# Performance work log

Measured on AMD Instinct MI355X. Metric: run time of the kernel, lower is better.

## Reference

```python
import jax, jax.numpy as jnp
import numpy as np

LENS = 0.4
DECAY = 0.2
THRESH = 0.2
LOG_SIG_MIN, LOG_SIG_MAX = -20.0, 2.0

# Surrogate-gradient spike: forward is heaviside, backward is rectangular window |x|<lens
@jax.custom_vjp
def act_fun(x):
    return (x > 0.0).astype(x.dtype)

def _act_fwd(x):
    return act_fun(x), x

def _act_bwd(x, g):
    return (g * (jnp.abs(x) < LENS).astype(g.dtype),)

act_fun.defvjp(_act_fwd, _act_bwd)


def _xavier(k, shape):
    fan_out, fan_in = shape
    lim = float(np.sqrt(6.0 / (fan_in + fan_out)))
    return jax.random.uniform(k, shape, jnp.float32, -lim, lim)


def setup_inputs() -> dict:
    key = jax.random.key(0)
    ks = jax.random.split(key, 9)
    B, IN, H, A = 4096, 512, 2048, 32
    return {
        "state": jax.random.normal(ks[0], (B, 5, IN), jnp.float32),
        "W_lif": _xavier(ks[1], (H, IN)), "b_lif": jnp.zeros((H,), jnp.float32),
        "W11": _xavier(ks[2], (H, H)), "b11": jnp.zeros((H,), jnp.float32),
        "W12": _xavier(ks[3], (H, H)), "b12": jnp.zeros((H,), jnp.float32),
        "W21": _xavier(ks[4], (H, H)), "b21": jnp.zeros((H,), jnp.float32),
        "W22": _xavier(ks[5], (H, H)), "b22": jnp.zeros((H,), jnp.float32),
        "Wm": _xavier(ks[6], (A, H)), "bm": jnp.zeros((A,), jnp.float32),
        "Wls": _xavier(ks[7], (A, H)), "bls": jnp.zeros((A,), jnp.float32),
    }


def reference(state, W_lif, b_lif, W11, b11, W12, b12, W21, b21, W22, b22, Wm, bm, Wls, bls):
    x_seq = jnp.repeat(state, 3, axis=1)
    # precompute fc(x) for all steps in one GEMM: [B,15,H]
    fc = jnp.einsum('bti,hi->bth', x_seq, W_lif) + b_lif
    B, T, H = fc.shape

    def step(carry, fc_t):
        mem, spike = carry
        mem1 = mem * DECAY * (1.0 - spike) + fc_t
        spike1 = act_fun(mem1 - THRESH)
        return (mem1, spike1), spike1

    init = (jnp.zeros((B, H), fc.dtype), jnp.zeros((B, H), fc.dtype))
    _, spikes = jax.lax.scan(step, init, jnp.swapaxes(fc, 0, 1))  # [T,B,H]
    x = jnp.mean(spikes, axis=0)  # [B,H]

    x1 = jax.nn.relu(x @ W11.T + b11)
    x1 = jax.nn.relu(x1 @ W12.T + b12)
    mean = x1 @ Wm.T + bm

    x2 = jax.nn.relu(x @ W21.T + b21)
    x2 = jax.nn.relu(x2 @ W22.T + b22)
    log_std = jnp.clip(x2 @ Wls.T + bls, LOG_SIG_MIN, LOG_SIG_MAX)
    return mean, log_std
```

## Files before the change

kernel.cpp:

```cpp
#include <hip/hip_runtime.h>
#include <hip/hip_bf16.h>


typedef _Float16 f16;
using f32x4 = __attribute__((ext_vector_type(4))) float;
using f16x8 = __attribute__((ext_vector_type(8))) f16;

#define MFMA16(a, b, c) __builtin_amdgcn_mfma_f32_16x16x32_f16((a), (b), (c), 0, 0, 0)
#define VMW8()  asm volatile("s_waitcnt vmcnt(8)" ::: "memory")
#define VMW4()  asm volatile("s_waitcnt vmcnt(4)" ::: "memory")
#define VMW0()  asm volatile("s_waitcnt vmcnt(0)" ::: "memory")
#define LGKM0() asm volatile("s_waitcnt lgkmcnt(0)" ::: "memory")
#define BARRIER() __builtin_amdgcn_s_barrier()
#define SCHED0() __builtin_amdgcn_sched_barrier(0)

__device__ __forceinline__ void gload16(const void* g, void* l) {
  __builtin_amdgcn_global_load_lds(
      (const __attribute__((address_space(1))) unsigned int*)g,
      (__attribute__((address_space(3))) unsigned int*)l, 16, 0, 0);
}

__device__ __forceinline__ void cvt8(const float4& a, const float4& b, f16* dst) {
  f16x8 d;
  d[0] = (f16)a.x; d[1] = (f16)a.y; d[2] = (f16)a.z; d[3] = (f16)a.w;
  d[4] = (f16)b.x; d[5] = (f16)b.y; d[6] = (f16)b.z; d[7] = (f16)b.w;
  *(f16x8*)dst = d;
}

__global__ __launch_bounds__(256) void cvt2b_kernel(
    const float* __restrict__ s0, f16* __restrict__ d0, int n8a,
    const float* __restrict__ s1, f16* __restrict__ d1, int n8b)
{
  int i = blockIdx.x * 256 + threadIdx.x;
  const float* src; f16* dst; int k;
  if (i < n8a) { src = s0; dst = d0; k = i; }
  else { k = i - n8a; if (k >= n8b) return; src = s1; dst = d1; }
  const float4* s4 = (const float4*)src;
  float4 a = s4[(size_t)k * 2], b = s4[(size_t)k * 2 + 1];
  cvt8(a, b, dst + (size_t)k * 8);
}

__global__ __launch_bounds__(256) void cvt4_kernel(
    const float* __restrict__ w0, const float* __restrict__ w1,
    const float* __restrict__ w2, const float* __restrict__ w3,
    f16* __restrict__ dst)
{
  int i = blockIdx.x * 256 + threadIdx.x;
  int which = i >> 19, k = i & 524287;
  const float* src = (which == 0) ? w0 : (which == 1) ? w1 : (which == 2) ? w2 : w3;
  const float4* s4 = (const float4*)src;
  float4 a = s4[(size_t)k * 2], b = s4[(size_t)k * 2 + 1];
  cvt8(a, b, dst + (size_t)i * 8);
}

__global__ __launch_bounds__(256) void cvt2_kernel(
    const float* __restrict__ s0, const float* __restrict__ s1,
    f16* __restrict__ d0, f16* __restrict__ d1, int n8each)
{
  int i = blockIdx.x * 256 + threadIdx.x;
  const float* src = (i < n8each) ? s0 : s1;
  f16* dst = (i < n8each) ? d0 : d1;
  int k = (i < n8each) ? i : i - n8each;
  if (k >= n8each) return;
  const float4* s4 = (const float4*)src;
  float4 a = s4[(size_t)k * 2], b = s4[(size_t)k * 2 + 1];
  cvt8(a, b, dst + (size_t)k * 8);
}

__global__ __launch_bounds__(512, 1) void lif256_kernel(
    const f16* __restrict__ S,
    const f16* __restrict__ W,
    const float* __restrict__ bl,
    f16* __restrict__ X)
{
  __shared__ alignas(16) f16 lds[6][128 * 64];

  const int tid = threadIdx.x, wid = tid >> 6, lane = tid & 63;
  const int wg = ((int)blockIdx.x % 8) * 64 + (int)blockIdx.x / 8;
  const int bn = wg & 15, bm = wg >> 4;
  const int b0 = bm * 128, h0 = bn * 128;
  const int wr0 = (wid >> 2) * 64, wc0 = (wid & 3) * 32;
  const int fr = lane & 15, fq = lane >> 4;
  const int sr = tid >> 3, scb = (tid & 7) * 16;

  f32x4 acc[4][2] = {};
  float mem[4][2][4] = {};
  float cnt[4][2][4] = {};

  char* Lb = (char*)&lds[0][0];
  const int xsw = (fr & 7) << 4;
  const int x0 = (fq * 16) ^ xsw;
  const int x1 = (64 + fq * 16) ^ xsw;
  char* const pA0 = Lb + (wr0 + fr) * 128 + x0;
  char* const pA1 = Lb + (wr0 + fr) * 128 + x1;
  char* const pB0 = Lb + 49152 + (wc0 + fr) * 128 + x0;
  char* const pB1 = Lb + 49152 + (wc0 + fr) * 128 + x1;

  const f16* sBase[2]; const f16* wBase[2];
#pragma unroll
  for (int l = 0; l < 2; ++l) {
    const int row = l * 64 + sr;
    const int c2 = scb ^ ((row & 7) << 4);
    sBase[l] = S + (size_t)(b0 + row) * 2560 + (c2 >> 1);
    wBase[l] = W + (size_t)(h0 + row) * 512 + (c2 >> 1);
  }

  auto STAGE = [&](int soSt, int g) {
    const int koff = (g >> 3) * 512 + (g & 7) * 64;
    const int kw = (g & 7) * 64;
#pragma unroll
    for (int l = 0; l < 2; ++l)
      gload16(sBase[l] + koff, Lb + soSt + l * 8192 + tid * 16);
#pragma unroll
    for (int l = 0; l < 2; ++l)
      gload16(wBase[l] + kw, Lb + 49152 + soSt + l * 8192 + tid * 16);
  };

  const float bias[2] = { bl[h0 + wc0 + fr], bl[h0 + wc0 + 16 + fr] };

  STAGE(0, 0);
  STAGE(16384, 1);
  VMW4();
  BARRIER();
  SCHED0();

  int soRead = 0, soStage = 32768;
  for (int g = 0; g < 40; ++g) {
    if (g + 2 < 40) STAGE(soStage, g + 2);
    SCHED0();

    f16x8 b[2][2], a0[2][2], a1[2][2];
#pragma unroll
    for (int nf = 0; nf < 2; ++nf) {
      b[nf][0] = *(const f16x8*)(pB0 + soRead + nf * 2048);
      b[nf][1] = *(const f16x8*)(pB1 + soRead + nf * 2048);
    }
#pragma unroll
    for (int i = 0; i < 2; ++i) {
      a0[i][0] = *(const f16x8*)(pA0 + soRead + i * 2048);
      a0[i][1] = *(const f16x8*)(pA1 + soRead + i * 2048);
      a1[i][0] = *(const f16x8*)(pA0 + soRead + (2 + i) * 2048);
      a1[i][1] = *(const f16x8*)(pA1 + soRead + (2 + i) * 2048);
    }

    __builtin_amdgcn_s_setprio(1);
#pragma unroll
    for (int i = 0; i < 2; ++i)
#pragma unroll
      for (int nf = 0; nf < 2; ++nf) {
        acc[i][nf] = MFMA16(a0[i][0], b[nf][0], acc[i][nf]);
        acc[i][nf] = MFMA16(a0[i][1], b[nf][1], acc[i][nf]);
      }
#pragma unroll
    for (int i = 0; i < 2; ++i)
#pragma unroll
      for (int nf = 0; nf < 2; ++nf) {
        acc[2 + i][nf] = MFMA16(a1[i][0], b[nf][0], acc[2 + i][nf]);
        acc[2 + i][nf] = MFMA16(a1[i][1], b[nf][1], acc[2 + i][nf]);
      }
    __builtin_amdgcn_s_setprio(0);

    if ((g & 7) == 7) {
#pragma unroll
      for (int mf = 0; mf < 4; ++mf)
#pragma unroll
        for (int nf = 0; nf < 2; ++nf) {
#pragma unroll
          for (int r = 0; r < 4; ++r) {
            const float fc = acc[mf][nf][r] + bias[nf];
            float m = mem[mf][nf][r], c = cnt[mf][nf][r];
#pragma unroll
            for (int j = 0; j < 3; ++j) {
              m = ((m > 0.2f) ? 0.f : m * 0.2f) + fc;
              c += (m > 0.2f) ? 1.f : 0.f;
            }
            mem[mf][nf][r] = m; cnt[mf][nf][r] = c;
          }
          acc[mf][nf] = f32x4{0.f, 0.f, 0.f, 0.f};
        }
    }

    LGKM0();
    if (g + 2 < 40)      { VMW4(); }
    else if (g + 1 < 40) { VMW0(); }
    BARRIER();
    SCHED0();

    soRead  = (soRead  == 32768) ? 0 : soRead  + 16384;
    soStage = (soStage == 32768) ? 0 : soStage + 16384;
  }

#pragma unroll
  for (int nf = 0; nf < 2; ++nf) {
    const int col = h0 + wc0 + nf * 16 + fr;
#pragma unroll
    for (int mf = 0; mf < 4; ++mf) {
      const int row0 = b0 + wr0 + mf * 16 + fq * 4;
#pragma unroll
      for (int r = 0; r < 4; ++r)
        X[(size_t)(row0 + r) * 2048 + col] = (f16)(cnt[mf][nf][r] / 15.0f);
    }
  }
}

__global__ __launch_bounds__(512, 2) void trunk256_kernel(
    const f16* __restrict__ A0, const f16* __restrict__ A1, int lda,
    const f16* __restrict__ W0, const f16* __restrict__ W1,
    const float* __restrict__ bb0, const float* __restrict__ bb1,
    f16* __restrict__ C0, f16* __restrict__ C1, int ldc,
    int nbm, int nbn_half, int K)
{
  __shared__ alignas(16) f16 lds[4][256 * 64];

  const int tid = threadIdx.x, wid = tid >> 6, lane = tid & 63;
  const int nwg = nbm * nbn_half * 2, q8 = nwg / 8;
  const int wg = ((int)blockIdx.x % 8) * q8 + (int)blockIdx.x / 8;
  const int bmi = wg % nbm, t = wg / nbm;
  const int half = (t >= nbn_half);
  const f16* Ap = half ? A1 : A0;
  const f16* Wp = half ? W1 : W0;
  const float* bias = half ? bb1 : bb0;
  f16* C = half ? C1 : C0;
  const int bm0 = bmi * 256;
  const int bn0 = (half ? t - nbn_half : t) * 256;

  const int wr0 = (wid >> 2) * 128, wc0 = (wid & 3) * 64;
  const int fr = lane & 15, fq = lane >> 4;
  const int sr = tid >> 3, scb = (tid & 7) * 16;

  f32x4 acc[8][4] = {};
  const int NT = K / 64;

  char* Lb = (char*)&lds[0][0];
  const int xsw = (fr & 7) << 4;
  const int x0 = (fq * 16) ^ xsw;
  const int x1 = (64 + fq * 16) ^ xsw;
  char* const pA0 = Lb + (wr0 + fr) * 128 + x0;
  char* const pA1 = Lb + (wr0 + fr) * 128 + x1;
  char* const pB0 = Lb + 65536 + (wc0 + fr) * 128 + x0;
  char* const pB1 = Lb + 65536 + (wc0 + fr) * 128 + x1;

  const f16* aBase[4]; const f16* wBase[4];
#pragma unroll
  for (int l = 0; l < 4; ++l) {
    const int row = l * 64 + sr;
    const int c2 = scb ^ ((row & 7) << 4);
    aBase[l] = Ap + (size_t)(bm0 + row) * lda + (c2 >> 1);
    wBase[l] = Wp + (size_t)(bn0 + row) * K + (c2 >> 1);
  }

  auto STAGE_A = [&](int slot, int kt) {
    const int koff = kt * 64;
#pragma unroll
    for (int l = 0; l < 4; ++l)
      gload16(aBase[l] + koff, Lb + slot * 32768 + l * 8192 + tid * 16);
  };
  auto STAGE_B = [&](int slot, int kt) {
    const int koff = kt * 64;
#pragma unroll
    for (int l = 0; l < 4; ++l)
      gload16(wBase[l] + koff, Lb + 65536 + slot * 32768 + l * 8192 + tid * 16);
  };

  STAGE_A(0, 0); STAGE_B(0, 0);
  STAGE_A(1, 1); STAGE_B(1, 1);
  VMW8();
  BARRIER();
  SCHED0();

#pragma unroll 2
  for (int kt = 0; kt < NT; ++kt) {
    const int slot = kt & 1;
    const int so = slot * 32768;

    auto QUAD = [&](int mbase, f16x8 (&b)[4][2], f16x8 (&a)[2][2]) {
      __builtin_amdgcn_s_setprio(1);
#pragma unroll
      for (int nf = 0; nf < 4; ++nf) {
        acc[mbase][nf]     = MFMA16(a[0][0], b[nf][0], acc[mbase][nf]);
        acc[mbase][nf]     = MFMA16(a[0][1], b[nf][1], acc[mbase][nf]);
        acc[mbase + 1][nf] = MFMA16(a[1][0], b[nf][0], acc[mbase + 1][nf]);
        acc[mbase + 1][nf] = MFMA16(a[1][1], b[nf][1], acc[mbase + 1][nf]);
      }
      __builtin_amdgcn_s_setprio(0);
    };

    f16x8 b[4][2], a0[2][2], a1[2][2];
#pragma unroll
    for (int nf = 0; nf < 4; ++nf) {
      b[nf][0] = *(const f16x8*)(pB0 + so + nf * 2048);
      b[nf][1] = *(const f16x8*)(pB1 + so + nf * 2048);
    }
#pragma unroll
    for (int i = 0; i < 2; ++i) {
      a0[i][0] = *(const f16x8*)(pA0 + so + i * 2048);
      a0[i][1] = *(const f16x8*)(pA1 + so + i * 2048);
    }
    LGKM0();
    BARRIER();
    if (kt + 2 < NT) STAGE_B(slot, kt + 2);
    SCHED0();

#pragma unroll
    for (int i = 0; i < 2; ++i) {
      a1[i][0] = *(const f16x8*)(pA0 + so + (2 + i) * 2048);
      a1[i][1] = *(const f16x8*)(pA1 + so + (2 + i) * 2048);
    }
    QUAD(0, b, a0);
    LGKM0(); SCHED0();
#pragma unroll
    for (int i = 0; i < 2; ++i) {
      a0[i][0] = *(const f16x8*)(pA0 + so + (4 + i) * 2048);
      a0[i][1] = *(const f16x8*)(pA1 + so + (4 + i) * 2048);
    }
    QUAD(2, b, a1);
    LGKM0(); SCHED0();
#pragma unroll
    for (int i = 0; i < 2; ++i) {
      a1[i][0] = *(const f16x8*)(pA0 + so + (6 + i) * 2048);
      a1[i][1] = *(const f16x8*)(pA1 + so + (6 + i) * 2048);
    }
    QUAD(4, b, a0);
    LGKM0();
    BARRIER();
    if (kt + 2 < NT) STAGE_A(slot, kt + 2);
    SCHED0();
    QUAD(6, b, a1);
    if (kt + 2 < NT)      { VMW8(); }
    else if (kt + 1 < NT) { VMW0(); }
    BARRIER();
    SCHED0();
  }

#pragma unroll
  for (int nf = 0; nf < 4; ++nf) {
    const int col = bn0 + wc0 + nf * 16 + fr;
    const float bv = bias[col];
#pragma unroll
    for (int m = 0; m < 8; ++m) {
      const int row0 = bm0 + wr0 + m * 16 + fq * 4;
#pragma unroll
      for (int r = 0; r < 4; ++r) {
        float v = fmaxf(acc[m][nf][r] + bv, 0.f);
        C[(size_t)(row0 + r) * ldc + col] = (f16)v;
      }
    }
  }
}

__global__ __launch_bounds__(256) void head_kernel(
    const f16* __restrict__ H1, const f16* __restrict__ H2,
    const f16* __restrict__ Wm, const float* __restrict__ bm,
    const f16* __restrict__ Wls, const float* __restrict__ bls,
    float* __restrict__ OUT, int M, int K)
{
  const int tid = threadIdx.x, wid = tid >> 6, lane = tid & 63;
  const int m0 = blockIdx.x * 64 + wid * 16;
  const int kb = (lane >> 4) * 8, fr = lane & 15, fq = lane >> 4;

  f32x4 a1[2] = {}, a2[2] = {};
  for (int k0 = 0; k0 < K; k0 += 32) {
    f16x8 f1 = *(const f16x8*)&H1[(size_t)(m0 + fr) * K + k0 + kb];
    f16x8 f2 = *(const f16x8*)&H2[(size_t)(m0 + fr) * K + k0 + kb];
#pragma unroll
    for (int n = 0; n < 2; ++n) {
      f16x8 wm = *(const f16x8*)&Wm[(size_t)(n * 16 + fr) * K + k0 + kb];
      f16x8 wl = *(const f16x8*)&Wls[(size_t)(n * 16 + fr) * K + k0 + kb];
      a1[n] = MFMA16(f1, wm, a1[n]);
      a2[n] = MFMA16(f2, wl, a2[n]);
    }
  }

#pragma unroll
  for (int n = 0; n < 2; ++n) {
    const int col = n * 16 + fr;
    const float bvm = bm[col];
    const float bvl = bls[col];
#pragma unroll
    for (int r = 0; r < 4; ++r) {
      const int row = m0 + fq * 4 + r;
      OUT[(size_t)row * 32 + col] = a1[n][r] + bvm;
      float lv = a2[n][r] + bvl;
      OUT[(size_t)M * 32 + (size_t)row * 32 + col] = fminf(fmaxf(lv, -20.f), 2.f);
    }
  }
}

extern "C" void kernel_launch(void* const* d_in, const int* in_sizes, int n_in,
                              void* d_out, int out_size, void* d_ws, size_t ws_size,
                              hipStream_t stream) {
  const float* state = (const float*)d_in[0];
  const float* W_lif = (const float*)d_in[1];
  const float* b_lif = (const float*)d_in[2];
  const float* W11   = (const float*)d_in[3];
  const float* b11   = (const float*)d_in[4];
  const float* W12   = (const float*)d_in[5];
  const float* b12   = (const float*)d_in[6];
  const float* W21   = (const float*)d_in[7];
  const float* b21   = (const float*)d_in[8];
  const float* W22   = (const float*)d_in[9];
  const float* b22   = (const float*)d_in[10];
  const float* Wm    = (const float*)d_in[11];
  const float* bm    = (const float*)d_in[12];
  const float* Wls   = (const float*)d_in[13];
  const float* bls   = (const float*)d_in[14];
  float* out = (float*)d_out;

  const int B = 4096, IN = 512, H = 2048;
  char* ws = (char*)d_ws;
  f16* x    = (f16*)(ws);
  f16* h1   = (f16*)(ws + 16777216);
  f16* h2   = (f16*)(ws + 33554432);
  f16* s16  = (f16*)(ws + 50331648);
  f16* wl16 = (f16*)(ws + 71303168);
  f16* w4   = (f16*)(ws + 50331648);
  f16* w11h = (f16*)(ws + 50331648);
  f16* w21h = (f16*)(ws + 58720256);
  f16* w12h = (f16*)(ws + 67108864);
  f16* w22h = (f16*)(ws + 75497472);
  f16* h22  = (f16*)(ws + 50331648);
  f16* wmh  = (f16*)(ws + 67108864);
  f16* wlsh = (f16*)(ws + 67239936);
  f16* h12  = x;

  const int n8s = B * 5 * IN / 8, n8w = H * IN / 8;
  cvt2b_kernel<<<(n8s + n8w + 255) / 256, 256, 0, stream>>>(
      state, s16, n8s, W_lif, wl16, n8w);

  lif256_kernel<<<512, 512, 0, stream>>>(s16, wl16, b_lif, x);

  cvt4_kernel<<<4 * 524288 / 256, 256, 0, stream>>>(W11, W21, W12, W22, w4);

  trunk256_kernel<<<256, 512, 0, stream>>>(x, x, H, w11h, w21h, b11, b21,
                                           h1, h2, H, 16, 8, H);
  trunk256_kernel<<<256, 512, 0, stream>>>(h1, h2, H, w12h, w22h, b12, b22,
                                           h12, h22, H, 16, 8, H);

  cvt2_kernel<<<2 * (32 * H / 8) / 256, 256, 0, stream>>>(Wm, Wls, wmh, wlsh, 32 * H / 8);
  head_kernel<<<B / 64, 256, 0, stream>>>(h12, h22, wmh, bm, wlsh, bls, out, B, H);
}
```

Baseline: 265.0 us.

## Enlarge LIF GEMM tile to 256x128 per block and pack spike counts

The LIF kernel's block tile grows from 128x128 to 256x128, so each wave computes a 64x64 sub-tile and each loaded B fragment is reused across four A fragments. Fewer blocks are launched (256 instead of 512), which cuts redundant W_lif loads and raises MFMA work per LDS read. Spike counts are packed as four 8-bit fields in one unsigned per fragment to save registers. In exchange, LDS use grows to 144KB and register pressure rises, and the smaller grid may underfill the CUs.

```diff
diff --git a/kernel.cpp b/kernel.cpp
--- a/kernel.cpp
+++ b/kernel.cpp
@@ -8,7 +8,7 @@
 
 #define MFMA16(a, b, c) __builtin_amdgcn_mfma_f32_16x16x32_f16((a), (b), (c), 0, 0, 0)
 #define VMW8()  asm volatile("s_waitcnt vmcnt(8)" ::: "memory")
-#define VMW4()  asm volatile("s_waitcnt vmcnt(4)" ::: "memory")
+#define VMW6()  asm volatile("s_waitcnt vmcnt(6)" ::: "memory")
 #define VMW0()  asm volatile("s_waitcnt vmcnt(0)" ::: "memory")
 #define LGKM0() asm volatile("s_waitcnt lgkmcnt(0)" ::: "memory")
 #define BARRIER() __builtin_amdgcn_s_barrier()
@@ -73,90 +73,88 @@
     const float* __restrict__ bl,
     f16* __restrict__ X)
 {
-  __shared__ alignas(16) f16 lds[6][128 * 64];
+  __shared__ alignas(16) f16 lds[73728];
 
   const int tid = threadIdx.x, wid = tid >> 6, lane = tid & 63;
-  const int wg = ((int)blockIdx.x % 8) * 64 + (int)blockIdx.x / 8;
+  const int wg = ((int)blockIdx.x % 8) * 32 + (int)blockIdx.x / 8;
   const int bn = wg & 15, bm = wg >> 4;
-  const int b0 = bm * 128, h0 = bn * 128;
-  const int wr0 = (wid >> 2) * 64, wc0 = (wid & 3) * 32;
+  const int b0 = bm * 256, h0 = bn * 128;
+  const int wr0 = (wid >> 1) * 64, wc0 = (wid & 1) * 64;
   const int fr = lane & 15, fq = lane >> 4;
   const int sr = tid >> 3, scb = (tid & 7) * 16;
 
-  f32x4 acc[4][2] = {};
-  float mem[4][2][4] = {};
-  float cnt[4][2][4] = {};
-
-  char* Lb = (char*)&lds[0][0];
+  f32x4 acc[4][4] = {};
+  float mem[4][4][4] = {};
+  unsigned pcnt[4][4] = {};
+
+  char* Lb = (char*)&lds[0];
   const int xsw = (fr & 7) << 4;
   const int x0 = (fq * 16) ^ xsw;
   const int x1 = (64 + fq * 16) ^ xsw;
   char* const pA0 = Lb + (wr0 + fr) * 128 + x0;
   char* const pA1 = Lb + (wr0 + fr) * 128 + x1;
-  char* const pB0 = Lb + 49152 + (wc0 + fr) * 128 + x0;
-  char* const pB1 = Lb + 49152 + (wc0 + fr) * 128 + x1;
-
-  const f16* sBase[2]; const f16* wBase[2];
+  char* const pB0 = Lb + 98304 + (wc0 + fr) * 128 + x0;
+  char* const pB1 = Lb + 98304 + (wc0 + fr) * 128 + x1;
+
+  const f16* sBase[4]; const f16* wBase[2];
+#pragma unroll
+  for (int l = 0; l < 4; ++l) {
+    const int row = l * 64 + sr;
+    const int c2 = scb ^ ((row & 7) << 4);
+    sBase[l] = S + (size_t)(b0 + row) * 2560 + (c2 >> 1);
+  }
 #pragma unroll
   for (int l = 0; l < 2; ++l) {
     const int row = l * 64 + sr;
     const int c2 = scb ^ ((row & 7) << 4);
-    sBase[l] = S + (size_t)(b0 + row) * 2560 + (c2 >> 1);
     wBase[l] = W + (size_t)(h0 + row) * 512 + (c2 >> 1);
   }
 
-  auto STAGE = [&](int soSt, int g) {
+  auto STAGE = [&](int soA, int soB, int g) {
     const int koff = (g >> 3) * 512 + (g & 7) * 64;
     const int kw = (g & 7) * 64;
 #pragma unroll
+    for (int l = 0; l < 4; ++l)
+      gload16(sBase[l] + koff, Lb + soA + l * 8192 + tid * 16);
+#pragma unroll
     for (int l = 0; l < 2; ++l)
-      gload16(sBase[l] + koff, Lb + soSt + l * 8192 + tid * 16);
-#pragma unroll
-    for (int l = 0; l < 2; ++l)
-      gload16(wBase[l] + kw, Lb + 49152 + soSt + l * 8192 + tid * 16);
+      gload16(wBase[l] + kw, Lb + 98304 + soB + l * 8192 + tid * 16);
   };
 
-  const float bias[2] = { bl[h0 + wc0 + fr], bl[h0 + wc0 + 16 + fr] };
-
-  STAGE(0, 0);
-  STAGE(16384, 1);
-  VMW4();
+  const float bias[4] = { bl[h0 + wc0 + fr],      bl[h0 + wc0 + 16 + fr],
+                          bl[h0 + wc0 + 32 + fr], bl[h0 + wc0 + 48 + fr] };
+
+  STAGE(0, 0, 0);
+  STAGE(32768, 16384, 1);
+  VMW6();
   BARRIER();
   SCHED0();
 
-  int soRead = 0, soStage = 32768;
+  int soA = 0, soB = 0;
+  int soStA = 65536, soStB = 32768;
   for (int g = 0; g < 40; ++g) {
-    if (g + 2 < 40) STAGE(soStage, g + 2);
+    if (g + 2 < 40) STAGE(soStA, soStB, g + 2);
     SCHED0();
 
-    f16x8 b[2][2], a0[2][2], a1[2][2];
-#pragma unroll
-    for (int nf = 0; nf < 2; ++nf) {
-      b[nf][0] = *(const f16x8*)(pB0 + soRead + nf * 2048);
-      b[nf][1] = *(const f16x8*)(pB1 + soRead + nf * 2048);
-    }
-#pragma unroll
-    for (int i = 0; i < 2; ++i) {
-      a0[i][0] = *(const f16x8*)(pA0 + soRead + i * 2048);
-      a0[i][1] = *(const f16x8*)(pA1 + soRead + i * 2048);
-      a1[i][0] = *(const f16x8*)(pA0 + soRead + (2 + i) * 2048);
-      a1[i][1] = *(const f16x8*)(pA1 + soRead + (2 + i) * 2048);
+    f16x8 b[4][2], a[4][2];
+#pragma unroll
+    for (int nf = 0; nf < 4; ++nf) {
+      b[nf][0] = *(const f16x8*)(pB0 + soB + nf * 2048);
+      b[nf][1] = *(const f16x8*)(pB1 + soB + nf * 2048);
+    }
+#pragma unroll
+    for (int mf = 0; mf < 4; ++mf) {
+      a[mf][0] = *(const f16x8*)(pA0 + soA + mf * 2048);
+      a[mf][1] = *(const f16x8*)(pA1 + soA + mf * 2048);
     }
 
     __builtin_amdgcn_s_setprio(1);
 #pragma unroll
-    for (int i = 0; i < 2; ++i)
-#pragma unroll
-      for (int nf = 0; nf < 2; ++nf) {
-        acc[i][nf] = MFMA16(a0[i][0], b[nf][0], acc[i][nf]);
-        acc[i][nf] = MFMA16(a0[i][1], b[nf][1], acc[i][nf]);
-      }
-#pragma unroll
-    for (int i = 0; i < 2; ++i)
-#pragma unroll
-      for (int nf = 0; nf < 2; ++nf) {
-        acc[2 + i][nf] = MFMA16(a1[i][0], b[nf][0], acc[2 + i][nf]);
-        acc[2 + i][nf] = MFMA16(a1[i][1], b[nf][1], acc[2 + i][nf]);
+    for (int mf = 0; mf < 4; ++mf)
+#pragma unroll
+      for (int nf = 0; nf < 4; ++nf) {
+        acc[mf][nf] = MFMA16(a[mf][0], b[nf][0], acc[mf][nf]);
+        acc[mf][nf] = MFMA16(a[mf][1], b[nf][1], acc[mf][nf]);
       }
     __builtin_amdgcn_s_setprio(0);
 
@@ -164,41 +162,48 @@
 #pragma unroll
       for (int mf = 0; mf < 4; ++mf)
 #pragma unroll
-        for (int nf = 0; nf < 2; ++nf) {
+        for (int nf = 0; nf < 4; ++nf) {
+          unsigned pc = pcnt[mf][nf];
 #pragma unroll
           for (int r = 0; r < 4; ++r) {
             const float fc = acc[mf][nf][r] + bias[nf];
-            float m = mem[mf][nf][r], c = cnt[mf][nf][r];
+            float m = mem[mf][nf][r];
+            const unsigned inc = 1u << (8 * r);
 #pragma unroll
             for (int j = 0; j < 3; ++j) {
               m = ((m > 0.2f) ? 0.f : m * 0.2f) + fc;
-              c += (m > 0.2f) ? 1.f : 0.f;
+              pc += (m > 0.2f) ? inc : 0u;
             }
-            mem[mf][nf][r] = m; cnt[mf][nf][r] = c;
+            mem[mf][nf][r] = m;
           }
+          pcnt[mf][nf] = pc;
           acc[mf][nf] = f32x4{0.f, 0.f, 0.f, 0.f};
         }
     }
 
     LGKM0();
-    if (g + 2 < 40)      { VMW4(); }
+    if (g + 2 < 40)      { VMW6(); }
     else if (g + 1 < 40) { VMW0(); }
     BARRIER();
     SCHED0();
 
-    soRead  = (soRead  == 32768) ? 0 : soRead  + 16384;
-    soStage = (soStage == 32768) ? 0 : soStage + 16384;
-  }
-
-#pragma unroll
-  for (int nf = 0; nf < 2; ++nf) {
+    soA   = (soA   == 65536) ? 0 : soA   + 32768;
+    soB   = (soB   == 32768) ? 0 : soB   + 16384;
+    soStA = (soStA == 65536) ? 0 : soStA + 32768;
+    soStB = (soStB == 32768) ? 0 : soStB + 16384;
+  }
+
+#pragma unroll
+  for (int nf = 0; nf < 4; ++nf) {
     const int col = h0 + wc0 + nf * 16 + fr;
 #pragma unroll
     for (int mf = 0; mf < 4; ++mf) {
       const int row0 = b0 + wr0 + mf * 16 + fq * 4;
 #pragma unroll
-      for (int r = 0; r < 4; ++r)
-        X[(size_t)(row0 + r) * 2048 + col] = (f16)(cnt[mf][nf][r] / 15.0f);
+      for (int r = 0; r < 4; ++r) {
+        const float c = (float)((pcnt[mf][nf] >> (8 * r)) & 255u);
+        X[(size_t)(row0 + r) * 2048 + col] = (f16)(c / 15.0f);
+      }
     }
   }
 }
@@ -427,7 +432,7 @@
   cvt2b_kernel<<<(n8s + n8w + 255) / 256, 256, 0, stream>>>(
       state, s16, n8s, W_lif, wl16, n8w);
 
-  lif256_kernel<<<512, 512, 0, stream>>>(s16, wl16, b_lif, x);
+  lif256_kernel<<<256, 512, 0, stream>>>(s16, wl16, b_lif, x);
 
   cvt4_kernel<<<4 * 524288 / 256, 256, 0, stream>>>(W11, W21, W12, W22, w4);
 
```

Result: no change. 259.9 us (median of 2 runs) (-1.9%).
